# Optimization experiments

Hardware: AMD Instinct MI355X
Metric: run time of the kernel (lower is better)

The kernel has to match this reference:

```python
import jax, jax.numpy as jnp
from jax import lax
import numpy as np

B, INP, WIDTH, OUTP, E, H = 32, 1024, 256, 1024, 8, 14
EPS = 1e-5


def setup_inputs() -> dict:
    key = jax.random.key(0)
    ks = jax.random.split(key, 12)
    n = lambda k, s, sc=0.05: jax.random.normal(k, s, jnp.float32) * sc
    return {
        "x": jax.random.normal(ks[0], (B, INP, H, H), jnp.float32),
        "w1": n(ks[1], (E, WIDTH, INP, 1, 1)),
        "w2": n(ks[2], (E, WIDTH, WIDTH, 3, 3)),
        "w3": n(ks[3], (E, OUTP, WIDTH, 1, 1)),
        "r1_w": n(ks[4], (INP, E)), "r1_b": jnp.zeros((E,), jnp.float32),
        "r2_w": n(ks[5], (WIDTH, E)), "r2_b": jnp.zeros((E,), jnp.float32),
        "r3_w": n(ks[6], (WIDTH, E)), "r3_b": jnp.zeros((E,), jnp.float32),
        "bn1_g": jax.random.uniform(ks[7], (WIDTH,), jnp.float32, 0.5, 1.5),
        "bn1_b": n(ks[8], (WIDTH,), 0.1),
        "bn1_m": jnp.zeros((WIDTH,), jnp.float32), "bn1_v": jnp.ones((WIDTH,), jnp.float32),
        "bn2_g": jax.random.uniform(ks[9], (WIDTH,), jnp.float32, 0.5, 1.5),
        "bn2_b": n(ks[10], (WIDTH,), 0.1),
        "bn2_m": jnp.zeros((WIDTH,), jnp.float32), "bn2_v": jnp.ones((WIDTH,), jnp.float32),
        "bn3_g": jax.random.uniform(ks[11], (OUTP,), jnp.float32, 0.5, 1.5),
        "bn3_b": jnp.zeros((OUTP,), jnp.float32),
        "bn3_m": jnp.zeros((OUTP,), jnp.float32), "bn3_v": jnp.ones((OUTP,), jnp.float32),
    }


def _route(x, w, b):
    # global avg pool -> linear -> sigmoid : [B, E]
    return jax.nn.sigmoid(x.mean(axis=(2, 3)) @ w + b)


def _cond_conv(x, w, rw, stride=1, padding=0, dilation=1, groups=1):
    # x: [B,Cin,H,W]; w: [E,Cout,Cin/groups,kh,kw]; rw: [B,E]
    Bn, Cin, Hh, Ww = x.shape
    _, Cout, Cin_g, kh, kw = w.shape
    # per-sample expert-combined kernels, then batch-grouped conv
    cw = jnp.einsum('be,eoikl->boikl', rw, w).reshape(Bn * Cout, Cin_g, kh, kw)
    out = lax.conv_general_dilated(
        x.reshape(1, Bn * Cin, Hh, Ww), cw,
        window_strides=(stride, stride),
        padding=[(padding, padding), (padding, padding)],
        rhs_dilation=(dilation, dilation),
        feature_group_count=Bn * groups,
        dimension_numbers=('NCHW', 'OIHW', 'NCHW'))
    return out.reshape(Bn, Cout, out.shape[2], out.shape[3])


def _bn(x, g, b, m, v):
    inv = lax.rsqrt(v + EPS) * g
    return x * inv[None, :, None, None] + (b - m * inv)[None, :, None, None]


def reference(x, w1, w2, w3, r1_w, r1_b, r2_w, r2_b, r3_w, r3_b,
              bn1_g, bn1_b, bn1_m, bn1_v, bn2_g, bn2_b, bn2_m, bn2_v,
              bn3_g, bn3_b, bn3_m, bn3_v):
    identity = x
    rw1 = _route(x, r1_w, r1_b)
    out = jax.nn.relu(_bn(_cond_conv(x, w1, rw1), bn1_g, bn1_b, bn1_m, bn1_v))
    rw2 = _route(out, r2_w, r2_b)
    out = jax.nn.relu(_bn(_cond_conv(out, w2, rw2, stride=1, padding=1), bn2_g, bn2_b, bn2_m, bn2_v))
    rw3 = _route(out, r3_w, r3_b)
    out = _bn(_cond_conv(out, w3, rw3), bn3_g, bn3_b, bn3_m, bn3_v)
    return jax.nn.relu(out + identity)
```

## Files before the change

kernel.cpp:

```cpp
#include <hip/hip_runtime.h>
#include <hip/hip_bf16.h>

#define BB 32
#define INP 1024
#define WIDTH 256
#define OUTP 1024
#define NE 8
#define HW 196
#define HH 14
#define EPS 1e-5f

#define S1 (WIDTH * INP)
#define S2 (WIDTH * WIDTH * 9)
#define S3 (OUTP * WIDTH)

typedef __attribute__((ext_vector_type(8))) short bf16x8;
typedef __attribute__((ext_vector_type(4))) float f32x4;
typedef __attribute__((ext_vector_type(8))) unsigned short u16x8;


__device__ __forceinline__ unsigned short f2bf_bits(float f) {
    unsigned u = __float_as_uint(f);
    u += 0x7FFFu + ((u >> 16) & 1u);
    return (unsigned short)(u >> 16);
}
__device__ __forceinline__ float bf2f(unsigned short h) {
    return __uint_as_float((unsigned)h << 16);
}

#if defined(__has_builtin)
#if __has_builtin(__builtin_amdgcn_global_load_lds)
#define HAVE_GLL 1
#endif
#endif
__device__ __forceinline__ void gl2lds(const unsigned short* g, unsigned short* l,
                                       int lane) {
#ifdef HAVE_GLL
    __builtin_amdgcn_global_load_lds(
        (const __attribute__((address_space(1))) unsigned int*)(const void*)g,
        (__attribute__((address_space(3))) unsigned int*)(void*)l, 16, 0, 0);
#else
    *(u16x8*)(l + lane * 8) = *(const u16x8*)g;
#endif
}

__device__ __forceinline__ void block_route(
    const float* __restrict__ vec, const float* __restrict__ W,
    const float* __restrict__ bias, float scale, int C, int g,
    float* srw, int tid) {
    int wv = tid >> 6, lane = tid & 63;
    float p0[NE], p1[NE];
#pragma unroll
    for (int e = 0; e < NE; e++) { p0[e] = 0.f; p1[e] = 0.f; }
    const float* v0 = vec + (size_t)(g * 8 + wv * 2) * C;
    const float* v1 = v0 + C;
    for (int c = lane; c < C; c += 64) {
        float4 wa = *(const float4*)(W + c * 8);
        float4 wb = *(const float4*)(W + c * 8 + 4);
        float m0 = v0[c], m1 = v1[c];
        p0[0] += m0 * wa.x; p0[1] += m0 * wa.y; p0[2] += m0 * wa.z; p0[3] += m0 * wa.w;
        p0[4] += m0 * wb.x; p0[5] += m0 * wb.y; p0[6] += m0 * wb.z; p0[7] += m0 * wb.w;
        p1[0] += m1 * wa.x; p1[1] += m1 * wa.y; p1[2] += m1 * wa.z; p1[3] += m1 * wa.w;
        p1[4] += m1 * wb.x; p1[5] += m1 * wb.y; p1[6] += m1 * wb.z; p1[7] += m1 * wb.w;
    }
#pragma unroll
    for (int j = 1; j < 64; j <<= 1) {
#pragma unroll
        for (int e = 0; e < NE; e++) {
            p0[e] += __shfl_xor(p0[e], j, 64);
            p1[e] += __shfl_xor(p1[e], j, 64);
        }
    }
    if (lane == 0) {
#pragma unroll
        for (int e = 0; e < NE; e++) {
            srw[(wv * 2) * 8 + e] = 1.0f / (1.0f + expf(-(scale * p0[e] + bias[e])));
            srw[(wv * 2 + 1) * 8 + e] = 1.0f / (1.0f + expf(-(scale * p1[e] + bias[e])));
        }
    }
    __syncthreads();
}

__global__ __launch_bounds__(256) void pre_kernel(
    const float* __restrict__ x, unsigned short* __restrict__ xb,
    float* __restrict__ mean1,
    const float* __restrict__ w2, unsigned short* __restrict__ wb2) {
    __shared__ __align__(16) char smem[128 * 17 * 4];
    int blk = blockIdx.x, t = threadIdx.x;
    if (blk < 256) {
        float (*lt)[17] = (float(*)[17])smem;
        int b = blk >> 3, yq = blk & 7, c0 = yq * 128;
        int cr = t >> 1, half = t & 1;
        const float* src = x + ((size_t)(b * INP + c0 + cr)) * HW;
        float msum = 0.f;
        int j = t >> 4, nl = t & 15;
        for (int pg = 0; pg < 14; pg++) {
            int p0 = pg * 16 + half * 8;
            float vv[8];
            if (pg < 12) {
                float4 a = *(const float4*)(src + p0);
                float4 c = *(const float4*)(src + p0 + 4);
                vv[0] = a.x; vv[1] = a.y; vv[2] = a.z; vv[3] = a.w;
                vv[4] = c.x; vv[5] = c.y; vv[6] = c.z; vv[7] = c.w;
            } else {
#pragma unroll
                for (int i = 0; i < 8; i++) {
                    int p = p0 + i;
                    vv[i] = (p < HW) ? src[p] : 0.f;
                }
            }
#pragma unroll
            for (int i = 0; i < 8; i++) { msum += vv[i]; lt[cr][half * 8 + i] = vv[i]; }
            __syncthreads();
            unsigned short pk[8];
#pragma unroll
            for (int i = 0; i < 8; i++) pk[i] = f2bf_bits(lt[j * 8 + i][nl]);
            size_t tile = ((size_t)b * 14 + pg) * 32 + (size_t)(yq * 4 + (j >> 2));
            int lane = nl | ((j & 3) << 4);
            *(u16x8*)(xb + tile * 512 + lane * 8) = *(u16x8*)pk;
            __syncthreads();
        }
        float other = __shfl_xor(msum, 1, 64);
        if (half == 0) mean1[b * INP + c0 + cr] = (msum + other) * (1.0f / (float)HW);
    } else {
        unsigned short* lds = (unsigned short*)smem;
        int eo = blk - 256;
        const float* src = w2 + (size_t)eo * 2304 + (size_t)t * 9;
#pragma unroll
        for (int t9 = 0; t9 < 9; t9++) lds[t9 * 256 + t] = f2bf_bits(src[t9]);
        __syncthreads();
        unsigned short* dst = wb2 + (size_t)eo * 2304;
        for (int j = t; j < 288; j += 256)
            *(u16x8*)(dst + j * 8) = *(const u16x8*)(lds + j * 8);
    }
}

__global__ __launch_bounds__(256) void combine_cont_r(
    const float* __restrict__ w, const float* __restrict__ vec,
    const float* __restrict__ rW, const float* __restrict__ rB, float scale, int C,
    unsigned short* __restrict__ cw, int S, int Mt, int Kt) {
    __shared__ float srw[64];
    int tid = threadIdx.x, wv = tid >> 6, lane = tid & 63, ml = lane & 15, k8l = lane >> 4;
    int g = blockIdx.y;
    block_route(vec, rW, rB, scale, C, g, srw, tid);
    int kq = Kt >> 2;
    int mt = blockIdx.x / kq, kt = (blockIdx.x - mt * kq) * 4 + wv;
    int K = Kt * 32;
    const float* src = w + (size_t)(mt * 16 + ml) * K + kt * 32 + k8l * 8;
    float v[NE][8];
#pragma unroll
    for (int e = 0; e < NE; e++) {
        float4 a = *(const float4*)(src + (size_t)e * S);
        float4 c = *(const float4*)(src + (size_t)e * S + 4);
        v[e][0] = a.x; v[e][1] = a.y; v[e][2] = a.z; v[e][3] = a.w;
        v[e][4] = c.x; v[e][5] = c.y; v[e][6] = c.z; v[e][7] = c.w;
    }
    size_t dto = ((size_t)mt * Kt + kt) * 512 + (size_t)lane * 8;
    size_t bstr = (size_t)Mt * Kt * 512;
    for (int bl = 0; bl < 8; bl++) {
        int b = g * 8 + bl;
        float acc[8];
#pragma unroll
        for (int jj = 0; jj < 8; jj++) acc[jj] = 0.f;
#pragma unroll
        for (int e = 0; e < NE; e++) {
            float r = srw[bl * NE + e];
#pragma unroll
            for (int jj = 0; jj < 8; jj++) acc[jj] += r * v[e][jj];
        }
        u16x8 o;
#pragma unroll
        for (int jj = 0; jj < 8; jj++) o[jj] = f2bf_bits(acc[jj]);
        *(u16x8*)(cw + (size_t)b * bstr + dto) = o;
    }
}

__global__ __launch_bounds__(256) void combine_w2_r(
    const unsigned short* __restrict__ wb2, const float* __restrict__ vec,
    const float* __restrict__ rW, const float* __restrict__ rB, float scale,
    unsigned short* __restrict__ cw) {
    __shared__ float srw[64];
    int tid = threadIdx.x, wv = tid >> 6, lane = tid & 63, ol = lane & 15, g4 = lane >> 4;
    int g = blockIdx.y;
    block_route(vec, rW, rB, scale, 256, g, srw, tid);
    int ot = blockIdx.x / 18, kt = (blockIdx.x - ot * 18) * 4 + wv;
    const unsigned short* src = wb2 + (size_t)(ot * 16 + ol) * 2304 + kt * 32 + g4 * 8;
    float v[NE][8];
#pragma unroll
    for (int e = 0; e < NE; e++) {
        u16x8 raw = *(const u16x8*)(src + (size_t)e * S2);
#pragma unroll
        for (int jj = 0; jj < 8; jj++) v[e][jj] = bf2f(raw[jj]);
    }
    size_t dto = ((size_t)ot * 72 + kt) * 512 + (size_t)lane * 8;
    for (int bl = 0; bl < 8; bl++) {
        int b = g * 8 + bl;
        float acc[8];
#pragma unroll
        for (int jj = 0; jj < 8; jj++) acc[jj] = 0.f;
#pragma unroll
        for (int e = 0; e < NE; e++) {
            float r = srw[bl * NE + e];
#pragma unroll
            for (int jj = 0; jj < 8; jj++) acc[jj] += r * v[e][jj];
        }
        u16x8 out;
#pragma unroll
        for (int jj = 0; jj < 8; jj++) out[jj] = f2bf_bits(acc[jj]);
        *(u16x8*)(cw + (size_t)b * (16 * 72 * 512) + dto) = out;
    }
}

__device__ __forceinline__ void epilogue_act(
    const f32x4* acc, int b, int mt, int nh, int lo, int g4,
    const float* __restrict__ g, const float* __restrict__ be,
    const float* __restrict__ mu, const float* __restrict__ var,
    unsigned short* __restrict__ actout, float* __restrict__ msum) {
    int c0 = mt * 16 + g4 * 4;
    float sc[4], sh[4];
#pragma unroll
    for (int r = 0; r < 4; r++) {
        float iv = rsqrtf(var[c0 + r] + EPS) * g[c0 + r];
        sc[r] = iv;
        sh[r] = be[c0 + r] - mu[c0 + r] * iv;
    }
    float ms[4] = {0.f, 0.f, 0.f, 0.f};
    int ktc = mt >> 1;
    int lanehi = ((mt * 2 + (g4 >> 1)) & 3) << 4;
#pragma unroll
    for (int t = 0; t < 7; t++) {
        int nt = nh * 7 + t;
        int n = nt * 16 + lo;
        float v[4];
#pragma unroll
        for (int r = 0; r < 4; r++) {
            float val = acc[t][r] * sc[r] + sh[r];
            val = fmaxf(val, 0.f);
            if (n >= HW) val = 0.f;
            v[r] = val;
            ms[r] += val;
        }
        unsigned p01 = (unsigned)f2bf_bits(v[0]) | ((unsigned)f2bf_bits(v[1]) << 16);
        unsigned p23 = (unsigned)f2bf_bits(v[2]) | ((unsigned)f2bf_bits(v[3]) << 16);
        size_t off = (((size_t)(b * 14 + nt)) * 8 + ktc) * 512 + (size_t)(lo | lanehi) * 8 + (g4 & 1) * 4;
        *(uint2*)(actout + off) = make_uint2(p01, p23);
    }
#pragma unroll
    for (int r = 0; r < 4; r++) {
        float s = ms[r];
        s += __shfl_xor(s, 1, 64);
        s += __shfl_xor(s, 2, 64);
        s += __shfl_xor(s, 4, 64);
        s += __shfl_xor(s, 8, 64);
        if (lo == 0) atomicAdd(&msum[b * 256 + c0 + r], s);
    }
}

__global__ __launch_bounds__(512) void gemm1_fused(
    const unsigned short* __restrict__ Bsw, const unsigned short* __restrict__ Asw,
    const float* __restrict__ g, const float* __restrict__ be,
    const float* __restrict__ mu, const float* __restrict__ var,
    unsigned short* __restrict__ actout, float* __restrict__ msum) {
    __shared__ __align__(16) unsigned short lAb[4][4 * 512];
    __shared__ __align__(16) unsigned short lBb[4][7 * 512];
    const int Kt = 32;
    int b = blockIdx.x, mh = blockIdx.y, nh = blockIdx.z;
    int tid = threadIdx.x, wv = tid >> 6, grp = wv >> 2, wl = wv & 3;
    int lane = tid & 63, lo = lane & 15, g4 = lane >> 4;
    const unsigned short* Ab = Asw + (size_t)(b * 16 + mh * 4) * Kt * 512;
    const unsigned short* Bb = Bsw + (size_t)(b * 14 + nh * 7) * Kt * 512;
    f32x4 acc[7];
#pragma unroll
    for (int t = 0; t < 7; t++) acc[t] = {0.f, 0.f, 0.f, 0.f};

    auto stage = [&](int kt, unsigned short* lA, unsigned short* lB) {
        gl2lds(Ab + ((size_t)wl * Kt + kt) * 512 + lane * 8, lA + wl * 512, lane);
        gl2lds(Bb + ((size_t)wl * Kt + kt) * 512 + lane * 8, lB + wl * 512, lane);
        if (wl < 3)
            gl2lds(Bb + ((size_t)(4 + wl) * Kt + kt) * 512 + lane * 8, lB + (4 + wl) * 512, lane);
    };
    auto compute = [&](const unsigned short* lA, const unsigned short* lB) {
        bf16x8 a0 = *(const bf16x8*)(lA + wl * 512 + lane * 8);
#pragma unroll
        for (int t = 0; t < 7; t++) {
            bf16x8 bt = *(const bf16x8*)(lB + t * 512 + lane * 8);
            acc[t] = __builtin_amdgcn_mfma_f32_16x16x32_bf16(a0, bt, acc[t], 0, 0, 0);
        }
    };

    stage(grp, lAb[grp], lBb[grp]);
    for (int kp = 0; kp < 16; kp++) {
        __syncthreads();
        if (kp < 15) {
            int s = 2 * kp + 2 + grp;
            stage(s, lAb[s & 3], lBb[s & 3]);
        }
        int c = (2 * kp + grp) & 3;
        compute(lAb[c], lBb[c]);
    }
    __syncthreads();
    float* red = (float*)&lBb[0][0];
    if (grp == 1) {
#pragma unroll
        for (int t = 0; t < 7; t++)
            *(f32x4*)(red + (((size_t)wl * 7 + t) * 64 + lane) * 4) = acc[t];
    }
    __syncthreads();
    if (grp == 0) {
#pragma unroll
        for (int t = 0; t < 7; t++) {
            f32x4 o = *(const f32x4*)(red + (((size_t)wl * 7 + t) * 64 + lane) * 4);
#pragma unroll
            for (int r = 0; r < 4; r++) acc[t][r] += o[r];
        }
        epilogue_act(acc, b, mh * 4 + wl, nh, lo, g4, g, be, mu, var, actout, msum);
    }
}

__global__ __launch_bounds__(512) void gemm2_fused(
    const unsigned short* __restrict__ act, const unsigned short* __restrict__ cw2,
    const unsigned short* __restrict__ zpad,
    const float* __restrict__ g, const float* __restrict__ be,
    const float* __restrict__ mu, const float* __restrict__ var,
    unsigned short* __restrict__ actout, float* __restrict__ msum) {
    __shared__ __align__(16) unsigned short lAb[4][4 * 512];
    __shared__ __align__(16) unsigned short lBb[4][7 * 512];
    int b = blockIdx.x, mh = blockIdx.y, nh = blockIdx.z;
    int tid = threadIdx.x, wv = tid >> 6, grp = wv >> 2, wl = wv & 3;
    int lane = tid & 63, lo = lane & 15, g4 = lane >> 4;
    const unsigned short* Ab = cw2 + (size_t)(b * 16 + mh * 4) * 72 * 512;
    const unsigned short* actb = act + (size_t)b * 14 * 8 * 512;

    int p0 = (nh * 7 + wl) * 16 + lo;
    int py0 = p0 / HH, px0 = p0 - (p0 / HH) * HH;
    bool pv0 = p0 < HW;
    int p1 = (nh * 7 + wl + 4) * 16 + lo;
    int py1 = p1 / HH, px1 = p1 - (p1 / HH) * HH;
    bool pv1 = (wl < 3) && (p1 < HW);

    f32x4 acc[7];
#pragma unroll
    for (int t = 0; t < 7; t++) acc[t] = {0.f, 0.f, 0.f, 0.f};

    auto stage = [&](int kt, unsigned short* lA, unsigned short* lB) {
        gl2lds(Ab + ((size_t)wl * 72 + kt) * 512 + lane * 8, lA + wl * 512, lane);
        int t9 = kt >> 3;
        int dy = t9 / 3 - 1, dx = t9 - (t9 / 3) * 3 - 1;
        int itile = kt & 7;
        {
            int sy = py0 + dy, sx = px0 + dx;
            bool ok = pv0 && sy >= 0 && sy < HH && sx >= 0 && sx < HH;
            int ns = sy * HH + sx;
            const unsigned short* gp = ok
                ? actb + ((size_t)(ns >> 4) * 8 + itile) * 512 + (size_t)((ns & 15) | (g4 << 4)) * 8
                : zpad;
            gl2lds(gp, lB + wl * 512, lane);
        }
        if (wl < 3) {
            int sy = py1 + dy, sx = px1 + dx;
            bool ok = pv1 && sy >= 0 && sy < HH && sx >= 0 && sx < HH;
            int ns = sy * HH + sx;
            const unsigned short* gp = ok
                ? actb + ((size_t)(ns >> 4) * 8 + itile) * 512 + (size_t)((ns & 15) | (g4 << 4)) * 8
                : zpad;
            gl2lds(gp, lB + (wl + 4) * 512, lane);
        }
    };
    auto compute = [&](const unsigned short* lA, const unsigned short* lB) {
        bf16x8 a0 = *(const bf16x8*)(lA + wl * 512 + lane * 8);
#pragma unroll
        for (int t = 0; t < 7; t++) {
            bf16x8 bt = *(const bf16x8*)(lB + t * 512 + lane * 8);
            acc[t] = __builtin_amdgcn_mfma_f32_16x16x32_bf16(a0, bt, acc[t], 0, 0, 0);
        }
    };

    stage(grp, lAb[grp], lBb[grp]);
    for (int kp = 0; kp < 36; kp++) {
        __syncthreads();
        if (kp < 35) {
            int s = 2 * kp + 2 + grp;
            stage(s, lAb[s & 3], lBb[s & 3]);
        }
        int c = (2 * kp + grp) & 3;
        compute(lAb[c], lBb[c]);
    }
    __syncthreads();
    float* red = (float*)&lBb[0][0];
    if (grp == 1) {
#pragma unroll
        for (int t = 0; t < 7; t++)
            *(f32x4*)(red + (((size_t)wl * 7 + t) * 64 + lane) * 4) = acc[t];
    }
    __syncthreads();
    if (grp == 0) {
#pragma unroll
        for (int t = 0; t < 7; t++) {
            f32x4 o = *(const f32x4*)(red + (((size_t)wl * 7 + t) * 64 + lane) * 4);
#pragma unroll
            for (int r = 0; r < 4; r++) acc[t][r] += o[r];
        }
        epilogue_act(acc, b, mh * 4 + wl, nh, lo, g4, g, be, mu, var, actout, msum);
    }
}

__global__ __launch_bounds__(512) void gemm3_fused(
    const unsigned short* __restrict__ Bsw, const unsigned short* __restrict__ Asw,
    const float* __restrict__ g, const float* __restrict__ be,
    const float* __restrict__ mu, const float* __restrict__ var,
    const unsigned short* __restrict__ xb, float* __restrict__ out) {
    __shared__ __align__(16) unsigned short lAb[4][8 * 512];
    __shared__ __align__(16) unsigned short lBb[4][7 * 512];
    int b = blockIdx.x, y = blockIdx.y, mh = y >> 1, nh = y & 1;
    int tid = threadIdx.x, wv = tid >> 6, grp = wv >> 2, wl = wv & 3;
    int lane = tid & 63, lo = lane & 15, g4 = lane >> 4;
    const unsigned short* Ab = Asw + (size_t)(b * 64 + mh * 8) * 8 * 512;
    const unsigned short* Bb = Bsw + (size_t)(b * 14 + nh * 7) * 8 * 512;
    f32x4 acc0[7], acc1[7];
#pragma unroll
    for (int t = 0; t < 7; t++) { acc0[t] = {0.f, 0.f, 0.f, 0.f}; acc1[t] = {0.f, 0.f, 0.f, 0.f}; }

    auto stage = [&](int kt, unsigned short* lA, unsigned short* lB) {
        gl2lds(Ab + ((size_t)wl * 8 + kt) * 512 + lane * 8, lA + wl * 512, lane);
        gl2lds(Ab + ((size_t)(wl + 4) * 8 + kt) * 512 + lane * 8, lA + (wl + 4) * 512, lane);
        gl2lds(Bb + ((size_t)wl * 8 + kt) * 512 + lane * 8, lB + wl * 512, lane);
        if (wl < 3)
            gl2lds(Bb + ((size_t)(4 + wl) * 8 + kt) * 512 + lane * 8, lB + (4 + wl) * 512, lane);
    };
    auto compute = [&](const unsigned short* lA, const unsigned short* lB) {
        bf16x8 a0 = *(const bf16x8*)(lA + wl * 512 + lane * 8);
        bf16x8 a1 = *(const bf16x8*)(lA + (wl + 4) * 512 + lane * 8);
#pragma unroll
        for (int t = 0; t < 7; t++) {
            bf16x8 bt = *(const bf16x8*)(lB + t * 512 + lane * 8);
            acc0[t] = __builtin_amdgcn_mfma_f32_16x16x32_bf16(a0, bt, acc0[t], 0, 0, 0);
            acc1[t] = __builtin_amdgcn_mfma_f32_16x16x32_bf16(a1, bt, acc1[t], 0, 0, 0);
        }
    };

    stage(grp, lAb[grp], lBb[grp]);
    for (int kp = 0; kp < 4; kp++) {
        __syncthreads();
        if (kp < 3) {
            int s = 2 * kp + 2 + grp;
            stage(s, lAb[s & 3], lBb[s & 3]);
        }
        int c = (2 * kp + grp) & 3;
        compute(lAb[c], lBb[c]);
    }
    __syncthreads();
    float* red = (float*)&lBb[0][0];
    if (grp == 1) {
#pragma unroll
        for (int t = 0; t < 7; t++)
            *(f32x4*)(red + (((size_t)wl * 7 + t) * 64 + lane) * 4) = acc0[t];
    }
    __syncthreads();
    if (grp == 0) {
#pragma unroll
        for (int t = 0; t < 7; t++) {
            f32x4 o = *(const f32x4*)(red + (((size_t)wl * 7 + t) * 64 + lane) * 4);
#pragma unroll
            for (int r = 0; r < 4; r++) acc0[t][r] += o[r];
        }
    }
    __syncthreads();
    if (grp == 1) {
#pragma unroll
        for (int t = 0; t < 7; t++)
            *(f32x4*)(red + (((size_t)wl * 7 + t) * 64 + lane) * 4) = acc1[t];
    }
    __syncthreads();
    if (grp != 0) return;
#pragma unroll
    for (int t = 0; t < 7; t++) {
        f32x4 o = *(const f32x4*)(red + (((size_t)wl * 7 + t) * 64 + lane) * 4);
#pragma unroll
        for (int r = 0; r < 4; r++) acc1[t][r] += o[r];
    }

#pragma unroll
    for (int a = 0; a < 2; a++) {
        int mt = mh * 8 + wl + 4 * a;
        int c0 = mt * 16 + g4 * 4;
        float sc[4], sh[4];
#pragma unroll
        for (int r = 0; r < 4; r++) {
            float iv = rsqrtf(var[c0 + r] + EPS) * g[c0 + r];
            sc[r] = iv;
            sh[r] = be[c0 + r] - mu[c0 + r] * iv;
        }
        int ktc = mt >> 1;
        int lanehi = ((mt * 2 + (g4 >> 1)) & 3) << 4;
#pragma unroll
        for (int t = 0; t < 7; t++) {
            int nt = nh * 7 + t;
            int n = nt * 16 + lo;
            if (n >= HW) continue;
            const unsigned short* xr = xb + (((size_t)(b * 14 + nt)) * 32 + ktc) * 512
                                       + (size_t)(lo | lanehi) * 8 + (g4 & 1) * 4;
            uint2 rv = *(const uint2*)xr;
            float res[4] = {bf2f((unsigned short)(rv.x & 0xffff)),
                            bf2f((unsigned short)(rv.x >> 16)),
                            bf2f((unsigned short)(rv.y & 0xffff)),
                            bf2f((unsigned short)(rv.y >> 16))};
            f32x4 av = a ? acc1[t] : acc0[t];
#pragma unroll
            for (int r = 0; r < 4; r++) {
                size_t oidx = ((size_t)(b * OUTP + c0 + r)) * HW + n;
                float val = av[r] * sc[r] + sh[r] + res[r];
                out[oidx] = fmaxf(val, 0.f);
            }
        }
    }
}

extern "C" void kernel_launch(void* const* d_in, const int* in_sizes, int n_in,
                              void* d_out, int out_size, void* d_ws, size_t ws_size,
                              hipStream_t stream) {
    const float* x    = (const float*)d_in[0];
    const float* w1   = (const float*)d_in[1];
    const float* w2   = (const float*)d_in[2];
    const float* w3   = (const float*)d_in[3];
    const float* r1_w = (const float*)d_in[4];
    const float* r1_b = (const float*)d_in[5];
    const float* r2_w = (const float*)d_in[6];
    const float* r2_b = (const float*)d_in[7];
    const float* r3_w = (const float*)d_in[8];
    const float* r3_b = (const float*)d_in[9];
    const float* bn1_g = (const float*)d_in[10];
    const float* bn1_b = (const float*)d_in[11];
    const float* bn1_m = (const float*)d_in[12];
    const float* bn1_v = (const float*)d_in[13];
    const float* bn2_g = (const float*)d_in[14];
    const float* bn2_b = (const float*)d_in[15];
    const float* bn2_m = (const float*)d_in[16];
    const float* bn2_v = (const float*)d_in[17];
    const float* bn3_g = (const float*)d_in[18];
    const float* bn3_b = (const float*)d_in[19];
    const float* bn3_m = (const float*)d_in[20];
    const float* bn3_v = (const float*)d_in[21];
    float* out = (float*)d_out;

    char* ws = (char*)d_ws;
    size_t off = 0;
    float* mean1 = (float*)(ws + off); off += (size_t)BB * INP * 4;
    float* msum2 = (float*)(ws + off); off += (size_t)BB * 256 * 4;
    float* msum3 = (float*)(ws + off); off += (size_t)BB * 256 * 4;
    unsigned short* zpad = (unsigned short*)(ws + off); off += 256;
    off = (off + 255) & ~(size_t)255;
    unsigned short* act1 = (unsigned short*)(ws + off); off += (size_t)BB * 14 * 8 * 512 * 2;
    unsigned short* act2 = (unsigned short*)(ws + off); off += (size_t)BB * 14 * 8 * 512 * 2;
    unsigned short* cw2 = (unsigned short*)(ws + off); off += (size_t)BB * 16 * 72 * 512 * 2;
    unsigned short* xb  = (unsigned short*)(ws + off); off += (size_t)BB * 14 * 32 * 512 * 2;
    unsigned short* wb2 = (unsigned short*)(ws + off); off += (size_t)S2 * NE * 2;
    unsigned short* cwX = (unsigned short*)(ws + off); off += (size_t)BB * S1 * 2;
    unsigned short* cw1 = cwX;
    unsigned short* cw3 = cwX;
    (void)ws_size;

    hipMemsetAsync(msum2, 0, (size_t)2 * BB * 256 * 4 + 256, stream);

    pre_kernel<<<2304, 256, 0, stream>>>(x, xb, mean1, w2, wb2);

    combine_cont_r<<<dim3(128, 4), 256, 0, stream>>>(w1, mean1, r1_w, r1_b, 1.0f, INP,
                                                     cw1, S1, 16, 32);
    gemm1_fused<<<dim3(BB, 4, 2), 512, 0, stream>>>(xb, cw1, bn1_g, bn1_b, bn1_m, bn1_v,
                                                    act1, msum2);

    combine_w2_r<<<dim3(288, 4), 256, 0, stream>>>(wb2, msum2, r2_w, r2_b,
                                                   1.0f / (float)HW, cw2);
    gemm2_fused<<<dim3(BB, 4, 2), 512, 0, stream>>>(act1, cw2, zpad, bn2_g, bn2_b,
                                                    bn2_m, bn2_v, act2, msum3);

    combine_cont_r<<<dim3(128, 4), 256, 0, stream>>>(w3, msum3, r3_w, r3_b,
                                                     1.0f / (float)HW, WIDTH,
                                                     cw3, S3, 64, 8);
    gemm3_fused<<<dim3(BB, 16), 512, 0, stream>>>(act2, cw3, bn3_g, bn3_b, bn3_m, bn3_v,
                                                  xb, out);
}
```

Measured before the change: 243.1 us.

## Deepen LDS prefetch pipeline with explicit vmcnt waits and raw barriers

All three fused GEMM kernels grow their LDS ring from 4 to 8 stages. Each wave group now keeps two K-tiles in flight instead of one, so global-to-LDS copies run further ahead of the MFMA work. Each `__syncthreads` is replaced by an explicit `s_waitcnt vmcnt(n)`, sized to the number of outstanding copies, plus a raw `s_barrier`, so the newest prefetch can stay in flight across the barrier. The cost is roughly double the shared memory per block. That may lower blocks per CU, and the hand-counted vmcnt values assume no other loads are outstanding.

```diff
diff --git a/kernel.cpp b/kernel.cpp
--- a/kernel.cpp
+++ b/kernel.cpp
@@ -18,6 +18,8 @@
 typedef __attribute__((ext_vector_type(4))) float f32x4;
 typedef __attribute__((ext_vector_type(8))) unsigned short u16x8;
 
+
+#define VMCNT(n) asm volatile("s_waitcnt vmcnt(" #n ")" ::: "memory")
 
 __device__ __forceinline__ unsigned short f2bf_bits(float f) {
     unsigned u = __float_as_uint(f);
@@ -261,8 +263,8 @@
     const float* __restrict__ g, const float* __restrict__ be,
     const float* __restrict__ mu, const float* __restrict__ var,
     unsigned short* __restrict__ actout, float* __restrict__ msum) {
-    __shared__ __align__(16) unsigned short lAb[4][4 * 512];
-    __shared__ __align__(16) unsigned short lBb[4][7 * 512];
+    __shared__ __align__(16) unsigned short lAb[8][4 * 512];
+    __shared__ __align__(16) unsigned short lBb[8][7 * 512];
     const int Kt = 32;
     int b = blockIdx.x, mh = blockIdx.y, nh = blockIdx.z;
     int tid = threadIdx.x, wv = tid >> 6, grp = wv >> 2, wl = wv & 3;
@@ -273,13 +275,17 @@
 #pragma unroll
     for (int t = 0; t < 7; t++) acc[t] = {0.f, 0.f, 0.f, 0.f};
 
-    auto stage = [&](int kt, unsigned short* lA, unsigned short* lB) {
+    auto stage = [&](int kt) {
+        unsigned short* lA = lAb[kt & 7];
+        unsigned short* lB = lBb[kt & 7];
         gl2lds(Ab + ((size_t)wl * Kt + kt) * 512 + lane * 8, lA + wl * 512, lane);
         gl2lds(Bb + ((size_t)wl * Kt + kt) * 512 + lane * 8, lB + wl * 512, lane);
         if (wl < 3)
             gl2lds(Bb + ((size_t)(4 + wl) * Kt + kt) * 512 + lane * 8, lB + (4 + wl) * 512, lane);
     };
-    auto compute = [&](const unsigned short* lA, const unsigned short* lB) {
+    auto compute = [&](int kt) {
+        const unsigned short* lA = lAb[kt & 7];
+        const unsigned short* lB = lBb[kt & 7];
         bf16x8 a0 = *(const bf16x8*)(lA + wl * 512 + lane * 8);
 #pragma unroll
         for (int t = 0; t < 7; t++) {
@@ -288,15 +294,19 @@
         }
     };
 
-    stage(grp, lAb[grp], lBb[grp]);
+    stage(grp);
+    stage(grp + 2);
     for (int kp = 0; kp < 16; kp++) {
-        __syncthreads();
-        if (kp < 15) {
-            int s = 2 * kp + 2 + grp;
-            stage(s, lAb[s & 3], lBb[s & 3]);
-        }
-        int c = (2 * kp + grp) & 3;
-        compute(lAb[c], lBb[c]);
+        int c = 2 * kp + grp;
+        if (c + 2 < 32) {
+            if (wl < 3) VMCNT(3); else VMCNT(2);
+        } else {
+            VMCNT(0);
+        }
+        __builtin_amdgcn_s_barrier();
+        int s = c + 4;
+        if (s < 32) stage(s);
+        compute(c);
     }
     __syncthreads();
     float* red = (float*)&lBb[0][0];
@@ -323,8 +333,8 @@
     const float* __restrict__ g, const float* __restrict__ be,
     const float* __restrict__ mu, const float* __restrict__ var,
     unsigned short* __restrict__ actout, float* __restrict__ msum) {
-    __shared__ __align__(16) unsigned short lAb[4][4 * 512];
-    __shared__ __align__(16) unsigned short lBb[4][7 * 512];
+    __shared__ __align__(16) unsigned short lAb[8][4 * 512];
+    __shared__ __align__(16) unsigned short lBb[8][7 * 512];
     int b = blockIdx.x, mh = blockIdx.y, nh = blockIdx.z;
     int tid = threadIdx.x, wv = tid >> 6, grp = wv >> 2, wl = wv & 3;
     int lane = tid & 63, lo = lane & 15, g4 = lane >> 4;
@@ -342,7 +352,9 @@
 #pragma unroll
     for (int t = 0; t < 7; t++) acc[t] = {0.f, 0.f, 0.f, 0.f};
 
-    auto stage = [&](int kt, unsigned short* lA, unsigned short* lB) {
+    auto stage = [&](int kt) {
+        unsigned short* lA = lAb[kt & 7];
+        unsigned short* lB = lBb[kt & 7];
         gl2lds(Ab + ((size_t)wl * 72 + kt) * 512 + lane * 8, lA + wl * 512, lane);
         int t9 = kt >> 3;
         int dy = t9 / 3 - 1, dx = t9 - (t9 / 3) * 3 - 1;
@@ -366,7 +378,9 @@
             gl2lds(gp, lB + (wl + 4) * 512, lane);
         }
     };
-    auto compute = [&](const unsigned short* lA, const unsigned short* lB) {
+    auto compute = [&](int kt) {
+        const unsigned short* lA = lAb[kt & 7];
+        const unsigned short* lB = lBb[kt & 7];
         bf16x8 a0 = *(const bf16x8*)(lA + wl * 512 + lane * 8);
 #pragma unroll
         for (int t = 0; t < 7; t++) {
@@ -375,15 +389,19 @@
         }
     };
 
-    stage(grp, lAb[grp], lBb[grp]);
+    stage(grp);
+    stage(grp + 2);
     for (int kp = 0; kp < 36; kp++) {
-        __syncthreads();
-        if (kp < 35) {
-            int s = 2 * kp + 2 + grp;
-            stage(s, lAb[s & 3], lBb[s & 3]);
-        }
-        int c = (2 * kp + grp) & 3;
-        compute(lAb[c], lBb[c]);
+        int c = 2 * kp + grp;
+        if (c + 2 < 72) {
+            if (wl < 3) VMCNT(3); else VMCNT(2);
+        } else {
+            VMCNT(0);
+        }
+        __builtin_amdgcn_s_barrier();
+        int s = c + 4;
+        if (s < 72) stage(s);
+        compute(c);
     }
     __syncthreads();
     float* red = (float*)&lBb[0][0];
@@ -409,8 +427,8 @@
     const float* __restrict__ g, const float* __restrict__ be,
     const float* __restrict__ mu, const float* __restrict__ var,
     const unsigned short* __restrict__ xb, float* __restrict__ out) {
-    __shared__ __align__(16) unsigned short lAb[4][8 * 512];
-    __shared__ __align__(16) unsigned short lBb[4][7 * 512];
+    __shared__ __align__(16) unsigned short lAb[8][8 * 512];
+    __shared__ __align__(16) unsigned short lBb[8][7 * 512];
     int b = blockIdx.x, y = blockIdx.y, mh = y >> 1, nh = y & 1;
     int tid = threadIdx.x, wv = tid >> 6, grp = wv >> 2, wl = wv & 3;
     int lane = tid & 63, lo = lane & 15, g4 = lane >> 4;
@@ -420,14 +438,18 @@
 #pragma unroll
     for (int t = 0; t < 7; t++) { acc0[t] = {0.f, 0.f, 0.f, 0.f}; acc1[t] = {0.f, 0.f, 0.f, 0.f}; }
 
-    auto stage = [&](int kt, unsigned short* lA, unsigned short* lB) {
+    auto stage = [&](int kt) {
+        unsigned short* lA = lAb[kt & 7];
+        unsigned short* lB = lBb[kt & 7];
         gl2lds(Ab + ((size_t)wl * 8 + kt) * 512 + lane * 8, lA + wl * 512, lane);
         gl2lds(Ab + ((size_t)(wl + 4) * 8 + kt) * 512 + lane * 8, lA + (wl + 4) * 512, lane);
         gl2lds(Bb + ((size_t)wl * 8 + kt) * 512 + lane * 8, lB + wl * 512, lane);
         if (wl < 3)
             gl2lds(Bb + ((size_t)(4 + wl) * 8 + kt) * 512 + lane * 8, lB + (4 + wl) * 512, lane);
     };
-    auto compute = [&](const unsigned short* lA, const unsigned short* lB) {
+    auto compute = [&](int kt) {
+        const unsigned short* lA = lAb[kt & 7];
+        const unsigned short* lB = lBb[kt & 7];
         bf16x8 a0 = *(const bf16x8*)(lA + wl * 512 + lane * 8);
         bf16x8 a1 = *(const bf16x8*)(lA + (wl + 4) * 512 + lane * 8);
 #pragma unroll
@@ -438,15 +460,19 @@
         }
     };
 
-    stage(grp, lAb[grp], lBb[grp]);
+    stage(grp);
+    stage(grp + 2);
     for (int kp = 0; kp < 4; kp++) {
-        __syncthreads();
-        if (kp < 3) {
-            int s = 2 * kp + 2 + grp;
-            stage(s, lAb[s & 3], lBb[s & 3]);
-        }
-        int c = (2 * kp + grp) & 3;
-        compute(lAb[c], lBb[c]);
+        int c = 2 * kp + grp;
+        if (c + 2 < 8) {
+            if (wl < 3) VMCNT(4); else VMCNT(3);
+        } else {
+            VMCNT(0);
+        }
+        __builtin_amdgcn_s_barrier();
+        int s = c + 4;
+        if (s < 8) stage(s);
+        compute(c);
     }
     __syncthreads();
     float* red = (float*)&lBb[0][0];
```

Measured after the change: 249.2 us. 2.5% more time.
